# Performance work log

Hardware: AMD Instinct MI355X
Metric: run time of the kernel (lower is better)

## Reference

```python
import jax, jax.numpy as jnp
import numpy as np

N_NODES = 100000
N_EDGES = 1600000
IN_DIM = 128
OUT_DIM = 32
LEAKY_SLOPE = 0.2  # tf.nn.leaky_relu default alpha
NEG_INF = -1e30


def setup_inputs() -> dict:
    key = jax.random.key(0)
    k1, k2, k3, k4, k5, k6 = jax.random.split(key, 6)
    node_embeddings = jax.random.normal(k1, (N_NODES, IN_DIM), dtype=jnp.float32)
    # glorot-uniform-like scaling for params
    W_n = jax.random.normal(k2, (IN_DIM, OUT_DIM), dtype=jnp.float32) * (1.0 / np.sqrt(IN_DIM))
    a_src = jax.random.normal(k3, (OUT_DIM,), dtype=jnp.float32) * (1.0 / np.sqrt(OUT_DIM))
    a_dst = jax.random.normal(k4, (OUT_DIM,), dtype=jnp.float32) * (1.0 / np.sqrt(OUT_DIM))
    src = jax.random.randint(k5, (N_EDGES,), 0, N_NODES, dtype=jnp.int32)
    dst = jnp.sort(jax.random.randint(k6, (N_EDGES,), 0, N_NODES, dtype=jnp.int32))
    return {"node_embeddings": node_embeddings, "W_n": W_n, "a_src": a_src,
            "a_dst": a_dst, "src": src, "dst": dst}


def reference(node_embeddings, W_n, a_src, a_dst, src, dst):
    # Linear transform: [n, d]
    z = node_embeddings @ W_n
    # Per-node attention scalars (z @ a_src / z @ a_dst), then gather per edge.
    s_src = z @ a_src  # [n]
    s_dst = z @ a_dst  # [n]
    e = jax.nn.leaky_relu(s_src[src] + s_dst[dst], negative_slope=LEAKY_SLOPE)  # [E]
    # Segment softmax over incoming edges of each dst node.
    e_max = jax.ops.segment_max(e, dst, num_segments=N_NODES, indices_are_sorted=True)
    e_max = jnp.where(jnp.isfinite(e_max), e_max, 0.0)  # zero-degree nodes
    e_exp = jnp.exp(e - e_max[dst])
    denom = jax.ops.segment_sum(e_exp, dst, num_segments=N_NODES, indices_are_sorted=True)
    alpha = e_exp / jnp.where(denom > 0, denom, 1.0)[dst]  # [E]
    # Weighted aggregation of src-transformed features onto dst.
    agg = jax.ops.segment_sum(alpha[:, None] * z[src], dst,
                              num_segments=N_NODES, indices_are_sorted=True)
    return jax.nn.relu(agg)  # [n, d]
```

## Files before the change

### kernel.cpp

```cpp
#include <hip/hip_runtime.h>
#include <math.h>

#define N_NODES 100000
#define N_EDGES 1600000
#define IN_DIM  128
#define OUT_DIM 32
#define LEAKY   0.2f

typedef unsigned int uint;
typedef unsigned short ushort;
typedef __attribute__((ext_vector_type(8))) short bf16x8;
typedef __attribute__((ext_vector_type(4))) float f32x4;

__device__ __forceinline__ ushort rne16(float f) {
    uint u = __float_as_uint(f);
    return (ushort)((u + 0x7fffu + ((u >> 16) & 1u)) >> 16);
}

__global__ __launch_bounds__(256) void gemm_s_kernel(
    const float* __restrict__ X, const float* __restrict__ W,
    const float* __restrict__ a_src, const float* __restrict__ a_dst,
    ushort* __restrict__ zu16, float* __restrict__ ssrc, float* __restrict__ sdst)
{
    const int lane = threadIdx.x & 63;
    const int wv   = threadIdx.x >> 6;
    const int m    = lane & 15;
    const int kg   = lane >> 4;

    const int rowA = blockIdx.x * 64 + wv * 16 + m;
    const int rA   = (rowA < N_NODES) ? rowA : (N_NODES - 1);
    const float* xp = X + (size_t)rA * IN_DIM + (kg << 3);

    float4 xA[4], xB[4];
    #pragma unroll
    for (int s = 0; s < 4; ++s) {
        xA[s] = *reinterpret_cast<const float4*>(xp + (s << 5));
        xB[s] = *reinterpret_cast<const float4*>(xp + (s << 5) + 4);
    }

    bf16x8 b0[4], b1[4];
    #pragma unroll
    for (int s = 0; s < 4; ++s) {
        #pragma unroll
        for (int j = 0; j < 8; ++j) {
            const int k = (s << 5) + (kg << 3) + j;
            b0[s][j] = (short)rne16(W[k * OUT_DIM + m]);
            b1[s][j] = (short)rne16(W[k * OUT_DIM + m + 16]);
        }
    }

    f32x4 acc0 = {0.f, 0.f, 0.f, 0.f};
    f32x4 acc1 = {0.f, 0.f, 0.f, 0.f};

    #pragma unroll
    for (int s = 0; s < 4; ++s) {
        float xs[8] = {xA[s].x, xA[s].y, xA[s].z, xA[s].w,
                       xB[s].x, xB[s].y, xB[s].z, xB[s].w};
        bf16x8 ah, al;
        #pragma unroll
        for (int j = 0; j < 8; ++j) {
            const uint u = __float_as_uint(xs[j]);
            ah[j] = (short)(u >> 16);
            const float lo = xs[j] - __uint_as_float(u & 0xffff0000u);
            al[j] = (short)(__float_as_uint(lo) >> 16);
        }
        acc0 = __builtin_amdgcn_mfma_f32_16x16x32_bf16(ah, b0[s], acc0, 0, 0, 0);
        acc0 = __builtin_amdgcn_mfma_f32_16x16x32_bf16(al, b0[s], acc0, 0, 0, 0);
        acc1 = __builtin_amdgcn_mfma_f32_16x16x32_bf16(ah, b1[s], acc1, 0, 0, 0);
        acc1 = __builtin_amdgcn_mfma_f32_16x16x32_bf16(al, b1[s], acc1, 0, 0, 0);
    }

    const float as0 = a_src[m], as1 = a_src[m + 16];
    const float ad0 = a_dst[m], ad1 = a_dst[m + 16];
    float ps[4], pd[4];
    #pragma unroll
    for (int r = 0; r < 4; ++r) {
        ps[r] = acc0[r] * as0 + acc1[r] * as1;
        pd[r] = acc0[r] * ad0 + acc1[r] * ad1;
    }
    #pragma unroll
    for (int r = 0; r < 4; ++r) {
        #pragma unroll
        for (int msk = 1; msk <= 8; msk <<= 1) {
            ps[r] += __shfl_xor(ps[r], msk, 64);
            pd[r] += __shfl_xor(pd[r], msk, 64);
        }
    }

    const int rbase = blockIdx.x * 64 + wv * 16 + (kg << 2);
    if (m == 0) {
        #pragma unroll
        for (int r = 0; r < 4; ++r)
            if (rbase + r < N_NODES) ssrc[rbase + r] = ps[r];
    }
    if (m == 1) {
        #pragma unroll
        for (int r = 0; r < 4; ++r)
            if (rbase + r < N_NODES) sdst[rbase + r] = pd[r];
    }

    #pragma unroll
    for (int r = 0; r < 4; ++r) {
        const int row = rbase + r;
        if (row < N_NODES) {
            zu16[row * OUT_DIM + m]      = rne16(acc0[r]);
            zu16[row * OUT_DIM + m + 16] = rne16(acc1[r]);
        }
    }
}

__global__ __launch_bounds__(256) void offsets_kernel(
    const int* __restrict__ dst, int* __restrict__ off)
{
    const int e = blockIdx.x * blockDim.x + threadIdx.x;
    if (e >= N_EDGES) return;
    const int d = dst[e];
    const int dprev = (e == 0) ? -1 : dst[e - 1];
    for (int n = dprev + 1; n <= d; ++n) off[n] = e;
    if (e == N_EDGES - 1) {
        for (int n = d + 1; n <= N_NODES; ++n) off[n] = N_EDGES;
    }
}

__global__ __launch_bounds__(256) void agg_kernel(
    const uint* __restrict__ zu, const float* __restrict__ ssrc,
    const float* __restrict__ sdst, const int* __restrict__ src,
    const int* __restrict__ off, float* __restrict__ out)
{
    __shared__ float2 sw[8][64];
    const int t = threadIdx.x;
    const int g = t >> 5, c = t & 31;
    const int n = blockIdx.x * 8 + g;
    if (n >= N_NODES) return;

    const int lo = off[n], hi = off[n + 1];
    const float sd = sdst[n];
    const int eh = c >> 2;
    const int ci = c & 3;

    float a0 = 0.f, a1 = 0.f, a2 = 0.f, a3 = 0.f;
    float a4 = 0.f, a5 = 0.f, a6 = 0.f, a7 = 0.f;
    float den = 0.f;

    for (int base = lo; base < hi; base += 32) {
        const int cnt = min(32, hi - base);
        sw[g][cnt + c] = make_float2(0.f, __int_as_float(0));
        if (c < cnt) {
            const int e = base + c;
            const int s = src[e];
            float x = ssrc[s] + sd;
            x = (x > 0.f) ? x : LEAKY * x;
            const float v = __expf(x);
            den += v;
            sw[g][c] = make_float2(v, __int_as_float(s << 4));
        }
        const float2 p0 = sw[g][eh];
        const float2 p1 = sw[g][8 + eh];
        const float2 p2 = sw[g][16 + eh];
        const float2 p3 = sw[g][24 + eh];
        const uint4 u0 = *reinterpret_cast<const uint4*>(zu + __float_as_int(p0.y) + (ci << 2));
        const uint4 u1 = *reinterpret_cast<const uint4*>(zu + __float_as_int(p1.y) + (ci << 2));
        const uint4 u2 = *reinterpret_cast<const uint4*>(zu + __float_as_int(p2.y) + (ci << 2));
        const uint4 u3 = *reinterpret_cast<const uint4*>(zu + __float_as_int(p3.y) + (ci << 2));
        #define ACC8(P, U)                                                  \
            a0 = fmaf(P.x, __uint_as_float(U.x << 16),         a0);         \
            a1 = fmaf(P.x, __uint_as_float(U.x & 0xffff0000u), a1);         \
            a2 = fmaf(P.x, __uint_as_float(U.y << 16),         a2);         \
            a3 = fmaf(P.x, __uint_as_float(U.y & 0xffff0000u), a3);         \
            a4 = fmaf(P.x, __uint_as_float(U.z << 16),         a4);         \
            a5 = fmaf(P.x, __uint_as_float(U.z & 0xffff0000u), a5);         \
            a6 = fmaf(P.x, __uint_as_float(U.w << 16),         a6);         \
            a7 = fmaf(P.x, __uint_as_float(U.w & 0xffff0000u), a7);
        ACC8(p0, u0) ACC8(p1, u1) ACC8(p2, u2) ACC8(p3, u3)
        #undef ACC8
    }

    #pragma unroll
    for (int msk = 4; msk <= 16; msk <<= 1) {
        a0 += __shfl_xor(a0, msk, 64); a1 += __shfl_xor(a1, msk, 64);
        a2 += __shfl_xor(a2, msk, 64); a3 += __shfl_xor(a3, msk, 64);
        a4 += __shfl_xor(a4, msk, 64); a5 += __shfl_xor(a5, msk, 64);
        a6 += __shfl_xor(a6, msk, 64); a7 += __shfl_xor(a7, msk, 64);
    }
    #pragma unroll
    for (int msk = 16; msk >= 1; msk >>= 1) den += __shfl_xor(den, msk, 64);

    if (eh == 0) {
        const float inv = (den > 0.f) ? (1.f / den) : 0.f;
        float4 o0, o1;
        o0.x = fmaxf(a0 * inv, 0.f); o0.y = fmaxf(a1 * inv, 0.f);
        o0.z = fmaxf(a2 * inv, 0.f); o0.w = fmaxf(a3 * inv, 0.f);
        o1.x = fmaxf(a4 * inv, 0.f); o1.y = fmaxf(a5 * inv, 0.f);
        o1.z = fmaxf(a6 * inv, 0.f); o1.w = fmaxf(a7 * inv, 0.f);
        float* op = &out[n * OUT_DIM + (ci << 3)];
        *reinterpret_cast<float4*>(op)     = o0;
        *reinterpret_cast<float4*>(op + 4) = o1;
    }
}

extern "C" void kernel_launch(void* const* d_in, const int* in_sizes, int n_in,
                              void* d_out, int out_size, void* d_ws, size_t ws_size,
                              hipStream_t stream) {
    const float* X     = (const float*)d_in[0];
    const float* W     = (const float*)d_in[1];
    const float* a_src = (const float*)d_in[2];
    const float* a_dst = (const float*)d_in[3];
    const int*   src   = (const int*)d_in[4];
    const int*   dst   = (const int*)d_in[5];
    float* out = (float*)d_out;

    char* ws = (char*)d_ws;
    ushort* zu16 = (ushort*)ws; ws += (size_t)N_NODES * OUT_DIM * sizeof(ushort);
    float* ssrc  = (float*)ws;  ws += (size_t)N_NODES * sizeof(float);
    float* sdst  = (float*)ws;  ws += (size_t)N_NODES * sizeof(float);
    int*   off   = (int*)ws;    ws += (size_t)(N_NODES + 1) * sizeof(int);

    offsets_kernel<<<(N_EDGES + 255) / 256, 256, 0, stream>>>(dst, off);
    gemm_s_kernel<<<(N_NODES + 63) / 64, 256, 0, stream>>>(X, W, a_src, a_dst, zu16, ssrc, sdst);
    agg_kernel<<<(N_NODES + 7) / 8, 256, 0, stream>>>((const uint*)zu16, ssrc, sdst, src, off, out);
}
```

Measured before the change: 49.39 us.

## Merge offsets computation into GEMM launch and stage bf16 W in LDS

The separate offsets kernel is folded into the GEMM kernel as extra blocks, so one launch runs both independent stages together. Inside each GEMM block, W is now loaded cooperatively, converted to bf16 once and kept transposed in shared memory. The per-lane scattered global loads and repeated conversions of W are replaced by vector LDS reads, and a_src/a_dst also come from shared memory. The cost is a __syncthreads and more shared memory per block, and the offsets blocks now carry the GEMM kernel's register and LDS footprint.

```diff
diff --git a/kernel.cpp b/kernel.cpp
--- a/kernel.cpp
+++ b/kernel.cpp
@@ -7,6 +7,9 @@
 #define OUT_DIM 32
 #define LEAKY   0.2f
 
+#define GEMM_NBLK 1563
+#define OFF_NBLK  6250
+
 typedef unsigned int uint;
 typedef unsigned short ushort;
 typedef __attribute__((ext_vector_type(8))) short bf16x8;
@@ -17,20 +20,37 @@
     return (ushort)((u + 0x7fffu + ((u >> 16) & 1u)) >> 16);
 }
 
-__global__ __launch_bounds__(256) void gemm_s_kernel(
+__global__ __launch_bounds__(256) void gemm_off_kernel(
     const float* __restrict__ X, const float* __restrict__ W,
     const float* __restrict__ a_src, const float* __restrict__ a_dst,
-    ushort* __restrict__ zu16, float* __restrict__ ssrc, float* __restrict__ sdst)
+    const int* __restrict__ dst,
+    ushort* __restrict__ zu16, float* __restrict__ ssrc, float* __restrict__ sdst,
+    int* __restrict__ off)
 {
-    const int lane = threadIdx.x & 63;
-    const int wv   = threadIdx.x >> 6;
+    __shared__ ushort WT[32][136];
+    __shared__ float asl[OUT_DIM], adl[OUT_DIM];
+
+    if (blockIdx.x >= GEMM_NBLK) {
+        const int e = (blockIdx.x - GEMM_NBLK) * 256 + threadIdx.x;
+        if (e >= N_EDGES) return;
+        const int d = dst[e];
+        const int dprev = (e == 0) ? -1 : dst[e - 1];
+        for (int n = dprev + 1; n <= d; ++n) off[n] = e;
+        if (e == N_EDGES - 1) {
+            for (int n = d + 1; n <= N_NODES; ++n) off[n] = N_EDGES;
+        }
+        return;
+    }
+
+    const int t    = threadIdx.x;
+    const int lane = t & 63;
+    const int wv   = t >> 6;
     const int m    = lane & 15;
     const int kg   = lane >> 4;
 
     const int rowA = blockIdx.x * 64 + wv * 16 + m;
     const int rA   = (rowA < N_NODES) ? rowA : (N_NODES - 1);
     const float* xp = X + (size_t)rA * IN_DIM + (kg << 3);
-
     float4 xA[4], xB[4];
     #pragma unroll
     for (int s = 0; s < 4; ++s) {
@@ -38,15 +58,27 @@
         xB[s] = *reinterpret_cast<const float4*>(xp + (s << 5) + 4);
     }
 
+    {
+        const int c = t & 31, kh = t >> 5;
+        uint pk[8];
+        #pragma unroll
+        for (int j2 = 0; j2 < 8; ++j2) {
+            const float w0 = W[(kh * 16 + 2 * j2)     * OUT_DIM + c];
+            const float w1 = W[(kh * 16 + 2 * j2 + 1) * OUT_DIM + c];
+            pk[j2] = (uint)rne16(w0) | ((uint)rne16(w1) << 16);
+        }
+        uint4* wd = reinterpret_cast<uint4*>(&WT[c][kh * 16]);
+        wd[0] = make_uint4(pk[0], pk[1], pk[2], pk[3]);
+        wd[1] = make_uint4(pk[4], pk[5], pk[6], pk[7]);
+        if (t < OUT_DIM) { asl[t] = a_src[t]; adl[t] = a_dst[t]; }
+    }
+    __syncthreads();
+
     bf16x8 b0[4], b1[4];
     #pragma unroll
     for (int s = 0; s < 4; ++s) {
-        #pragma unroll
-        for (int j = 0; j < 8; ++j) {
-            const int k = (s << 5) + (kg << 3) + j;
-            b0[s][j] = (short)rne16(W[k * OUT_DIM + m]);
-            b1[s][j] = (short)rne16(W[k * OUT_DIM + m + 16]);
-        }
+        b0[s] = *reinterpret_cast<bf16x8*>(&WT[m][(s << 5) + (kg << 3)]);
+        b1[s] = *reinterpret_cast<bf16x8*>(&WT[m + 16][(s << 5) + (kg << 3)]);
     }
 
     f32x4 acc0 = {0.f, 0.f, 0.f, 0.f};
@@ -70,8 +102,8 @@
         acc1 = __builtin_amdgcn_mfma_f32_16x16x32_bf16(al, b1[s], acc1, 0, 0, 0);
     }
 
-    const float as0 = a_src[m], as1 = a_src[m + 16];
-    const float ad0 = a_dst[m], ad1 = a_dst[m + 16];
+    const float as0 = asl[m], as1 = asl[m + 16];
+    const float ad0 = adl[m], ad1 = adl[m + 16];
     float ps[4], pd[4];
     #pragma unroll
     for (int r = 0; r < 4; ++r) {
@@ -106,19 +138,6 @@
             zu16[row * OUT_DIM + m]      = rne16(acc0[r]);
             zu16[row * OUT_DIM + m + 16] = rne16(acc1[r]);
         }
-    }
-}
-
-__global__ __launch_bounds__(256) void offsets_kernel(
-    const int* __restrict__ dst, int* __restrict__ off)
-{
-    const int e = blockIdx.x * blockDim.x + threadIdx.x;
-    if (e >= N_EDGES) return;
-    const int d = dst[e];
-    const int dprev = (e == 0) ? -1 : dst[e - 1];
-    for (int n = dprev + 1; n <= d; ++n) off[n] = e;
-    if (e == N_EDGES - 1) {
-        for (int n = d + 1; n <= N_NODES; ++n) off[n] = N_EDGES;
     }
 }
 
@@ -215,7 +234,7 @@
     float* sdst  = (float*)ws;  ws += (size_t)N_NODES * sizeof(float);
     int*   off   = (int*)ws;    ws += (size_t)(N_NODES + 1) * sizeof(int);
 
-    offsets_kernel<<<(N_EDGES + 255) / 256, 256, 0, stream>>>(dst, off);
-    gemm_s_kernel<<<(N_NODES + 63) / 64, 256, 0, stream>>>(X, W, a_src, a_dst, zu16, ssrc, sdst);
+    gemm_off_kernel<<<GEMM_NBLK + OFF_NBLK, 256, 0, stream>>>(
+        X, W, a_src, a_dst, dst, zu16, ssrc, sdst, off);
     agg_kernel<<<(N_NODES + 7) / 8, 256, 0, stream>>>((const uint*)zu16, ssrc, sdst, src, off, out);
 }
```

Measured after the change: 43.11 us. 12.7% less time.
